# Kernel optimization log

Measured on AMD Instinct MI355X. Metric: run time of the kernel, lower is better.

Reference implementation:

```python
import jax, jax.numpy as jnp
import numpy as np

B = 128; RES = 28; DIM = 192; HEADS = 6; WS = 7; HDIM = DIM // HEADS
NWIN = (RES // WS) ** 2; N = WS * WS; SCALE = HDIM ** -0.5

def _rel_pos_index():
    coords = np.stack(np.meshgrid(np.arange(WS), np.arange(WS), indexing='ij'))
    cf = coords.reshape(2, -1)
    rel = (cf[:, :, None] - cf[:, None, :]).transpose(1, 2, 0)
    rel[:, :, 0] += WS - 1; rel[:, :, 1] += WS - 1; rel[:, :, 0] *= 2 * WS - 1
    return jnp.asarray(rel.sum(-1))

RPI = _rel_pos_index()  # (49,49) int32

def gelu(x):
    return jax.nn.gelu(x, approximate=False)  # torch nn.GELU default (erf)

def ln(x, g, b, eps=1e-5):
    mu = jnp.mean(x, -1, keepdims=True)
    var = jnp.var(x, -1, keepdims=True)
    return (x - mu) * jax.lax.rsqrt(var + eps) * g + b

def feat_extract(x, dw, se1, se2, pw):
    # x: (B,C,H,W). depthwise3x3 -> GELU -> SE -> pointwise, residual, maxpool s2
    y = jax.lax.conv_general_dilated(x, dw, (1, 1), [(1, 1), (1, 1)],
                                     feature_group_count=DIM,
                                     dimension_numbers=('NCHW', 'OIHW', 'NCHW'))
    y = gelu(y)
    s = jnp.mean(y, (2, 3))                       # squeeze-excite
    s = jax.nn.sigmoid(gelu(s @ se1.T) @ se2.T)
    y = y * s[:, :, None, None]
    y = jax.lax.conv_general_dilated(y, pw, (1, 1), [(0, 0), (0, 0)],
                                     dimension_numbers=('NCHW', 'OIHW', 'NCHW'))
    x = x + y
    return jax.lax.reduce_window(x, -jnp.inf, jax.lax.max,
                                 (1, 1, 3, 3), (1, 1, 2, 2),
                                 [(0, 0), (0, 0), (1, 1), (1, 1)])

def win_part(x):
    b = x.shape[0]
    x = x.reshape(b, RES // WS, WS, RES // WS, WS, DIM).transpose(0, 1, 3, 2, 4, 5)
    return x.reshape(-1, N, DIM)

def win_rev(w, b):
    x = w.reshape(b, RES // WS, RES // WS, WS, WS, DIM).transpose(0, 1, 3, 2, 4, 5)
    return x.reshape(b, RES, RES, DIM)

def rel_bias(rpb):
    return jnp.take(rpb, RPI.reshape(-1), axis=0).reshape(N, N, HEADS).transpose(2, 0, 1)[None]

def attn_block(x, q_global, n1g, n1b, qkv_w, qkv_b, rpb, proj_w, proj_b,
               n2g, n2b, fc1w, fc1b, fc2w, fc2b, is_global):
    b = x.shape[0]
    xw = win_part(ln(x, n1g, n1b))                # (b*NWIN, N, C)
    B_ = xw.shape[0]
    if is_global:
        kv = (xw @ qkv_w.T + qkv_b).reshape(B_, N, 2, HEADS, HDIM).transpose(2, 0, 3, 1, 4)
        k, v = kv[0], kv[1]
        q = jnp.broadcast_to(q_global, (b, NWIN, HEADS, N, HDIM)).reshape(B_, HEADS, N, HDIM) * SCALE
    else:
        qkv = (xw @ qkv_w.T + qkv_b).reshape(B_, N, 3, HEADS, HDIM).transpose(2, 0, 3, 1, 4)
        q, k, v = qkv[0] * SCALE, qkv[1], qkv[2]
    attn = jnp.einsum('bhnd,bhmd->bhnm', q, k) + rel_bias(rpb)
    attn = jax.nn.softmax(attn, axis=-1)
    o = jnp.einsum('bhnm,bhmd->bhnd', attn, v).transpose(0, 2, 1, 3).reshape(B_, N, DIM)
    o = o @ proj_w.T + proj_b
    x = x + win_rev(o, b)
    h = ln(x, n2g, n2b)
    h = gelu(h @ fc1w.T + fc1b) @ fc2w.T + fc2b
    return x + h

def _forward(x, fe0_dw, fe0_se1, fe0_se2, fe0_pw, fe1_dw, fe1_se1, fe1_se2, fe1_pw,
             b0_n1g, b0_n1b, b0_qkv_w, b0_qkv_b, b0_rpb, b0_proj_w, b0_proj_b,
             b0_n2g, b0_n2b, b0_fc1w, b0_fc1b, b0_fc2w, b0_fc2b,
             b1_n1g, b1_n1b, b1_qkv_w, b1_qkv_b, b1_rpb, b1_proj_w, b1_proj_b,
             b1_n2g, b1_n2b, b1_fc1w, b1_fc1b, b1_fc2w, b1_fc2b):
    b = x.shape[0]
    # GlobalQueryGen: channel-first, two FeatExtract downsamples 28->14->7
    xc = jnp.transpose(x, (0, 3, 1, 2))
    xc = feat_extract(xc, fe0_dw, fe0_se1, fe0_se2, fe0_pw)
    xc = feat_extract(xc, fe1_dw, fe1_se1, fe1_se2, fe1_pw)
    qg = jnp.transpose(xc, (0, 2, 3, 1)).reshape(b, 1, N, HEADS, HDIM).transpose(0, 1, 3, 2, 4)
    # block 0: local window attention; block 1: global-query window attention
    x = attn_block(x, None, b0_n1g, b0_n1b, b0_qkv_w, b0_qkv_b, b0_rpb, b0_proj_w,
                   b0_proj_b, b0_n2g, b0_n2b, b0_fc1w, b0_fc1b, b0_fc2w, b0_fc2b, False)
    x = attn_block(x, qg, b1_n1g, b1_n1b, b1_qkv_w, b1_qkv_b, b1_rpb, b1_proj_w,
                   b1_proj_b, b1_n2g, b1_n2b, b1_fc1w, b1_fc1b, b1_fc2w, b1_fc2b, True)
    return x

def setup_inputs() -> dict:
    key = jax.random.key(0)
    ks = iter(jax.random.split(key, 64))
    r = lambda *s: jax.random.normal(next(ks), s, jnp.float32) * 0.02
    d = {'x': jax.random.normal(next(ks), (B, RES, RES, DIM), jnp.float32)}
    for i in range(2):
        d[f'fe{i}_dw'] = r(DIM, 1, 3, 3)
        d[f'fe{i}_se1'] = r(DIM // 4, DIM)
        d[f'fe{i}_se2'] = r(DIM, DIM // 4)
        d[f'fe{i}_pw'] = r(DIM, DIM, 1, 1)
    for i, qm in ((0, 3), (1, 2)):  # local: qkv, global: kv only
        p = f'b{i}_'
        d[p + 'n1g'] = jnp.ones(DIM, jnp.float32); d[p + 'n1b'] = jnp.zeros(DIM, jnp.float32)
        d[p + 'qkv_w'] = r(qm * DIM, DIM); d[p + 'qkv_b'] = r(qm * DIM)
        d[p + 'rpb'] = r((2 * WS - 1) ** 2, HEADS)
        d[p + 'proj_w'] = r(DIM, DIM); d[p + 'proj_b'] = r(DIM)
        d[p + 'n2g'] = jnp.ones(DIM, jnp.float32); d[p + 'n2b'] = jnp.zeros(DIM, jnp.float32)
        d[p + 'fc1w'] = r(4 * DIM, DIM); d[p + 'fc1b'] = r(4 * DIM)
        d[p + 'fc2w'] = r(DIM, 4 * DIM); d[p + 'fc2b'] = r(DIM)
    return d

def reference(x, fe0_dw, fe0_se1, fe0_se2, fe0_pw, fe1_dw, fe1_se1, fe1_se2, fe1_pw,
              b0_n1g, b0_n1b, b0_qkv_w, b0_qkv_b, b0_rpb, b0_proj_w, b0_proj_b,
              b0_n2g, b0_n2b, b0_fc1w, b0_fc1b, b0_fc2w, b0_fc2b,
              b1_n1g, b1_n1b, b1_qkv_w, b1_qkv_b, b1_rpb, b1_proj_w, b1_proj_b,
              b1_n2g, b1_n2b, b1_fc1w, b1_fc1b, b1_fc2w, b1_fc2b):
    return _forward(x, fe0_dw, fe0_se1, fe0_se2, fe0_pw, fe1_dw, fe1_se1, fe1_se2, fe1_pw,
                    b0_n1g, b0_n1b, b0_qkv_w, b0_qkv_b, b0_rpb, b0_proj_w, b0_proj_b,
                    b0_n2g, b0_n2b, b0_fc1w, b0_fc1b, b0_fc2w, b0_fc2b,
                    b1_n1g, b1_n1b, b1_qkv_w, b1_qkv_b, b1_rpb, b1_proj_w, b1_proj_b,
                    b1_n2g, b1_n2b, b1_fc1w, b1_fc1b, b1_fc2w, b1_fc2b)
```

## Files before the change

kernel.cpp:

```cpp
#include <hip/hip_runtime.h>
#include <hip/hip_bf16.h>
#include <math.h>

#define NB     128
#define RESX   28
#define DIMC   192
#define NHEADS 6
#define WSZ    7
#define HD     32
#define NTOK   49
#define SCALE  0.17677669529663687f
#define TOK28  (NB*RESX*RESX)
#define QSTR   208
#define VSTR   80
#define PSTR   80
#define HSTR   200
#define SEPARTS 8

typedef short    bf16x8 __attribute__((ext_vector_type(8)));
typedef float    f32x4  __attribute__((ext_vector_type(4)));

__device__ __forceinline__ float gelu_f(float x){
    return 0.5f * x * (1.0f + erff(x * 0.70710678118654752f));
}
__device__ __forceinline__ unsigned short f2bf(float f){
    unsigned int u = __float_as_uint(f);
    u += 0x7fffu + ((u >> 16) & 1u);
    return (unsigned short)(u >> 16);
}
__device__ __forceinline__ float bf2f(unsigned short u){
    return __uint_as_float(((unsigned int)u) << 16);
}
__device__ __forceinline__ bf16x8 pack8(float4 u, float4 v){
    bf16x8 r;
    r[0]=(short)f2bf(u.x); r[1]=(short)f2bf(u.y); r[2]=(short)f2bf(u.z); r[3]=(short)f2bf(u.w);
    r[4]=(short)f2bf(v.x); r[5]=(short)f2bf(v.y); r[6]=(short)f2bf(v.z); r[7]=(short)f2bf(v.w);
    return r;
}

__global__ __launch_bounds__(256) void ln_kernel(const float* __restrict__ x,
        const float* __restrict__ g, const float* __restrict__ be,
        float* __restrict__ out)
{
    int wid = threadIdx.x >> 6, lane = threadIdx.x & 63;
    size_t tok = (size_t)blockIdx.x * 4 + wid;
    const float* xr = x + tok * DIMC;
    float v0 = xr[lane], v1 = xr[lane + 64], v2 = xr[lane + 128];
    float s  = v0 + v1 + v2;
    float sq = v0*v0 + v1*v1 + v2*v2;
    #pragma unroll
    for (int o = 32; o > 0; o >>= 1){ s += __shfl_xor(s, o); sq += __shfl_xor(sq, o); }
    float mean = s * (1.0f/DIMC);
    float var  = sq * (1.0f/DIMC) - mean*mean;
    float rstd = rsqrtf(var + 1e-5f);
    float* orow = out + tok * DIMC;
    orow[lane]     = (v0-mean)*rstd*g[lane]     + be[lane];
    orow[lane+64]  = (v1-mean)*rstd*g[lane+64]  + be[lane+64];
    orow[lane+128] = (v2-mean)*rstd*g[lane+128] + be[lane+128];
}

__global__ __launch_bounds__(192) void dw_gelu_kernel(const float* __restrict__ x,
        const float* __restrict__ dw, float* __restrict__ y, int H, int W)
{
    __shared__ float wl[DIMC*9];
    int tx = threadIdx.x;
    #pragma unroll
    for (int q = 0; q < 9; ++q) wl[tx*9 + q] = dw[tx*9 + q];
    __syncthreads();
    int pix = tx / 48, c4 = tx - (tx/48)*48;
    int p = blockIdx.x*4 + pix;
    int w = p % W; int h = (p / W) % H; int b = p / (W*H);
    float wk[9][4];
    #pragma unroll
    for (int q = 0; q < 9; ++q){
        #pragma unroll
        for (int cc = 0; cc < 4; ++cc) wk[q][cc] = wl[(c4*4 + cc)*9 + q];
    }
    const float* base = x + (size_t)b*H*W*DIMC + c4*4;
    float4 acc = make_float4(0.f, 0.f, 0.f, 0.f);
    #pragma unroll
    for (int kh = 0; kh < 3; ++kh){
        int hh = h + kh - 1; if (hh < 0 || hh >= H) continue;
        #pragma unroll
        for (int kw = 0; kw < 3; ++kw){
            int ww = w + kw - 1; if (ww < 0 || ww >= W) continue;
            float4 v = *(const float4*)(base + ((size_t)hh*W + ww)*DIMC);
            int q = kh*3 + kw;
            acc.x += v.x*wk[q][0]; acc.y += v.y*wk[q][1];
            acc.z += v.z*wk[q][2]; acc.w += v.w*wk[q][3];
        }
    }
    float4 o;
    o.x = gelu_f(acc.x); o.y = gelu_f(acc.y);
    o.z = gelu_f(acc.z); o.w = gelu_f(acc.w);
    *(float4*)(y + (size_t)p*DIMC + c4*4) = o;
}

__global__ void se_reduce_kernel(const float* __restrict__ y, float* __restrict__ part,
                                 int HW)
{
    int blk = blockIdx.x;
    int b = blk / SEPARTS, i = blk - b*SEPARTS;
    int c = threadIdx.x;
    int chunk = (HW + SEPARTS - 1) / SEPARTS;
    int p0 = i*chunk, p1 = p0 + chunk;
    if (p1 > HW) p1 = HW;
    const float* base = y + (size_t)b*HW*DIMC + c;
    float acc = 0.f;
    for (int p = p0; p < p1; ++p) acc += base[(size_t)p*DIMC];
    part[(size_t)blk*DIMC + c] = acc;
}

__global__ void se_mlp_kernel(const float* __restrict__ part, const float* __restrict__ w1,
                              const float* __restrict__ w2, float* __restrict__ s, int HW)
{
    __shared__ float sl[DIMC];
    __shared__ float mid[48];
    int b = blockIdx.x; int t = threadIdx.x;
    float acc0 = 0.f;
    #pragma unroll
    for (int i = 0; i < SEPARTS; ++i)
        acc0 += part[((size_t)b*SEPARTS + i)*DIMC + t];
    sl[t] = acc0 / (float)HW;
    __syncthreads();
    if (t < 48){
        float acc = 0.f;
        for (int c = 0; c < DIMC; ++c) acc += sl[c] * w1[t*DIMC + c];
        mid[t] = gelu_f(acc);
    }
    __syncthreads();
    float acc = 0.f;
    #pragma unroll 8
    for (int j = 0; j < 48; ++j) acc += mid[j] * w2[t*48 + j];
    s[b*DIMC + t] = 1.0f / (1.0f + expf(-acc));
}

__global__ __launch_bounds__(192) void maxpool_kernel(const float* __restrict__ x,
        float* __restrict__ out, int H, int W)
{
    int H2 = H >> 1, W2 = W >> 1;
    int tx = threadIdx.x;
    int pix = tx / 48, c4 = tx - (tx/48)*48;
    int p = blockIdx.x*4 + pix;
    if (p >= NB*H2*W2) return;
    int w2 = p % W2; int h2 = (p / W2) % H2; int b = p / (W2*H2);
    const float* base = x + (size_t)b*H*W*DIMC + c4*4;
    float4 m = make_float4(-INFINITY, -INFINITY, -INFINITY, -INFINITY);
    #pragma unroll
    for (int dh = -1; dh <= 1; ++dh){
        int h = 2*h2 + dh; if (h < 0 || h >= H) continue;
        #pragma unroll
        for (int dw = -1; dw <= 1; ++dw){
            int w = 2*w2 + dw; if (w < 0 || w >= W) continue;
            float4 v = *(const float4*)(base + ((size_t)h*W + w)*DIMC);
            m.x = fmaxf(m.x, v.x); m.y = fmaxf(m.y, v.y);
            m.z = fmaxf(m.z, v.z); m.w = fmaxf(m.w, v.w);
        }
    }
    *(float4*)(out + (size_t)p*DIMC + c4*4) = m;
}

struct PackArgs {
    const float* src[8];
    unsigned short* dst[8];
    int K[8];
    int tEnd[8];
    int nseg;
};
__global__ __launch_bounds__(256) void pack_multi_kernel(PackArgs a)
{
    int t = blockIdx.x*256 + threadIdx.x;
    int seg = 0;
    while (seg < a.nseg && t >= a.tEnd[seg]) ++seg;
    if (seg >= a.nseg) return;
    int t0 = seg ? a.tEnd[seg-1] : 0;
    int tl = t - t0;
    int lane = tl & 63, frag = tl >> 6;
    int K = a.K[seg], ks = K >> 5;
    int j = frag / ks, s = frag - j*ks;
    const float* wr = a.src[seg] + (size_t)(j*16 + (lane & 15))*K + s*32 + ((lane>>4)<<3);
    bf16x8 r = pack8(*(const float4*)wr, *(const float4*)(wr + 4));
    *((bf16x8*)(a.dst[seg] + (size_t)tl*8)) = r;
}

__global__ __launch_bounds__(256) void gemmW_kernel(
    const float* __restrict__ in, const unsigned short* __restrict__ Wp,
    const float* __restrict__ bias, const float* __restrict__ res,
    float* __restrict__ out, int N, int M, int ppw,
    const float* __restrict__ sv, int HW)
{
    __shared__ __align__(16) unsigned short wlds[72*512];
    __shared__ __align__(16) float sbias[192];
    int tid = threadIdx.x;
    int l = tid & 63, w = tid >> 6, c = l & 15, g = l >> 4;
    int nc = blockIdx.y;
    const bf16x8* wsrc = (const bf16x8*)(Wp + (size_t)nc*36864);
    bf16x8* wdst = (bf16x8*)wlds;
    #pragma unroll 2
    for (int i = tid; i < 4608; i += 256) wdst[i] = wsrc[i];
    if (tid < 48){
        float4 bb = bias ? ((const float4*)(bias + nc*192))[tid]
                         : make_float4(0.f,0.f,0.f,0.f);
        ((float4*)sbias)[tid] = bb;
    }
    __syncthreads();
    size_t mbase = (size_t)blockIdx.x*(128*ppw) + (size_t)w*(32*ppw);
    for (int p = 0; p < ppw; ++p){
        size_t m0 = mbase + (size_t)p*32;
        if ((long)m0 >= M) break;
        bool st1 = (long)(m0 + 16) < M;
        const float* ar0 = in + (m0 + c)*DIMC;
        const float* ar1 = ar0 + 16*DIMC;
        bf16x8 b0[6], b1[6];
        #pragma unroll
        for (int s = 0; s < 6; ++s){
            int k0 = s*32 + g*8;
            float4 u0 = *(const float4*)(ar0 + k0), v0 = *(const float4*)(ar0 + k0 + 4);
            float4 u1 = *(const float4*)(ar1 + k0), v1 = *(const float4*)(ar1 + k0 + 4);
            if (sv){
                int bi0 = (int)((m0 + c)/HW), bi1 = (int)((m0 + 16 + c)/HW);
                float4 a0 = *(const float4*)(sv + (size_t)bi0*DIMC + k0);
                float4 a1 = *(const float4*)(sv + (size_t)bi0*DIMC + k0 + 4);
                float4 d0 = *(const float4*)(sv + (size_t)bi1*DIMC + k0);
                float4 d1 = *(const float4*)(sv + (size_t)bi1*DIMC + k0 + 4);
                u0.x*=a0.x; u0.y*=a0.y; u0.z*=a0.z; u0.w*=a0.w;
                v0.x*=a1.x; v0.y*=a1.y; v0.z*=a1.z; v0.w*=a1.w;
                u1.x*=d0.x; u1.y*=d0.y; u1.z*=d0.z; u1.w*=d0.w;
                v1.x*=d1.x; v1.y*=d1.y; v1.z*=d1.z; v1.w*=d1.w;
            }
            b0[s] = pack8(u0, v0);
            b1[s] = pack8(u1, v1);
        }
        #pragma unroll 2
        for (int j = 0; j < 12; ++j){
            float4 bb = *(const float4*)(sbias + j*16 + g*4);
            f32x4 a0 = {bb.x, bb.y, bb.z, bb.w};
            f32x4 a1 = a0;
            const bf16x8* wf = (const bf16x8*)wlds + (size_t)j*6*64 + l;
            #pragma unroll
            for (int s = 0; s < 6; ++s){
                bf16x8 wfr = wf[s*64];
                a0 = __builtin_amdgcn_mfma_f32_16x16x32_bf16(wfr, b0[s], a0, 0, 0, 0);
                a1 = __builtin_amdgcn_mfma_f32_16x16x32_bf16(wfr, b1[s], a1, 0, 0, 0);
            }
            int ncol = nc*192 + j*16 + g*4;
            size_t o0 = (m0 + c)*(size_t)N + ncol;
            size_t o1 = o0 + (size_t)16*N;
            float4 r0 = res ? *(const float4*)(res + o0) : make_float4(0.f,0.f,0.f,0.f);
            *(float4*)(out + o0) = make_float4(a0[0]+r0.x, a0[1]+r0.y, a0[2]+r0.z, a0[3]+r0.w);
            if (st1){
                float4 r1 = res ? *(const float4*)(res + o1) : make_float4(0.f,0.f,0.f,0.f);
                *(float4*)(out + o1) = make_float4(a1[0]+r1.x, a1[1]+r1.y, a1[2]+r1.z, a1[3]+r1.w);
            }
        }
    }
}

__global__ __launch_bounds__(256, 2) void mlp_mfma_kernel(
    const float* __restrict__ xln,
    const unsigned short* __restrict__ W1p, const float* __restrict__ b1,
    const unsigned short* __restrict__ W2p, const float* __restrict__ b2,
    float* __restrict__ xout)
{
    __shared__ __align__(16) unsigned short h[2][64*HSTR];
    int l = threadIdx.x & 63, w = threadIdx.x >> 6;
    int c = l & 15, g = l >> 4;
    size_t m0 = (size_t)blockIdx.x*64;
    bf16x8 bx[4][6];
    #pragma unroll
    for (int mt = 0; mt < 4; ++mt){
        const float* ar = xln + (m0 + mt*16 + c)*DIMC;
        #pragma unroll
        for (int s = 0; s < 6; ++s){
            int k0 = s*32 + g*8;
            bx[mt][s] = pack8(*(const float4*)(ar + k0), *(const float4*)(ar + k0 + 4));
        }
    }
    f32x4 acc[4][3];
    #pragma unroll
    for (int jj = 0; jj < 3; ++jj){
        float4 b4 = *(const float4*)(b2 + (3*w + jj)*16 + g*4);
        f32x4 v = {b4.x, b4.y, b4.z, b4.w};
        #pragma unroll
        for (int mt = 0; mt < 4; ++mt) acc[mt][jj] = v;
    }
    for (int ch = 0; ch < 4; ++ch){
        unsigned short* hb = &h[ch & 1][0];
        #pragma unroll
        for (int jj = 0; jj < 3; ++jj){
            int j = ch*12 + 3*w + jj;
            float4 b40 = *(const float4*)(b1 + j*16 + g*4);
            f32x4 a0 = {b40.x, b40.y, b40.z, b40.w};
            f32x4 a1 = a0, a2 = a0, a3 = a0;
            const bf16x8* wp = (const bf16x8*)(W1p + ((size_t)(j*6)*64 + l)*8);
            #pragma unroll
            for (int s = 0; s < 6; ++s){
                bf16x8 wfr = wp[s*64];
                a0 = __builtin_amdgcn_mfma_f32_16x16x32_bf16(wfr, bx[0][s], a0, 0, 0, 0);
                a1 = __builtin_amdgcn_mfma_f32_16x16x32_bf16(wfr, bx[1][s], a1, 0, 0, 0);
                a2 = __builtin_amdgcn_mfma_f32_16x16x32_bf16(wfr, bx[2][s], a2, 0, 0, 0);
                a3 = __builtin_amdgcn_mfma_f32_16x16x32_bf16(wfr, bx[3][s], a3, 0, 0, 0);
            }
            int fb = (3*w + jj)*16 + g*4;
            ushort4 u;
            u.x=f2bf(gelu_f(a0[0])); u.y=f2bf(gelu_f(a0[1]));
            u.z=f2bf(gelu_f(a0[2])); u.w=f2bf(gelu_f(a0[3]));
            *(ushort4*)(hb + (0*16 + c)*HSTR + fb) = u;
            u.x=f2bf(gelu_f(a1[0])); u.y=f2bf(gelu_f(a1[1]));
            u.z=f2bf(gelu_f(a1[2])); u.w=f2bf(gelu_f(a1[3]));
            *(ushort4*)(hb + (1*16 + c)*HSTR + fb) = u;
            u.x=f2bf(gelu_f(a2[0])); u.y=f2bf(gelu_f(a2[1]));
            u.z=f2bf(gelu_f(a2[2])); u.w=f2bf(gelu_f(a2[3]));
            *(ushort4*)(hb + (2*16 + c)*HSTR + fb) = u;
            u.x=f2bf(gelu_f(a3[0])); u.y=f2bf(gelu_f(a3[1]));
            u.z=f2bf(gelu_f(a3[2])); u.w=f2bf(gelu_f(a3[3]));
            *(ushort4*)(hb + (3*16 + c)*HSTR + fb) = u;
        }
        __syncthreads();
        #pragma unroll
        for (int s = 0; s < 6; ++s){
            bf16x8 hf[4];
            #pragma unroll
            for (int mt = 0; mt < 4; ++mt)
                hf[mt] = *(const bf16x8*)(hb + (mt*16 + c)*HSTR + s*32 + g*8);
            #pragma unroll
            for (int jj = 0; jj < 3; ++jj){
                int j = 3*w + jj;
                bf16x8 wf = *(const bf16x8*)(W2p + ((size_t)(j*24 + ch*6 + s)*64 + l)*8);
                #pragma unroll
                for (int mt = 0; mt < 4; ++mt)
                    acc[mt][jj] = __builtin_amdgcn_mfma_f32_16x16x32_bf16(wf, hf[mt], acc[mt][jj], 0, 0, 0);
            }
        }
    }
    #pragma unroll
    for (int mt = 0; mt < 4; ++mt){
        #pragma unroll
        for (int jj = 0; jj < 3; ++jj){
            size_t o = (m0 + mt*16 + c)*DIMC + (3*w + jj)*16 + g*4;
            float4 r = *(const float4*)(xout + o);
            *(float4*)(xout + o) = make_float4(acc[mt][jj][0]+r.x, acc[mt][jj][1]+r.y,
                                               acc[mt][jj][2]+r.z, acc[mt][jj][3]+r.w);
        }
    }
}

__global__ __launch_bounds__(512, 2) void attn_fused_kernel(
    float* __restrict__ xio, const unsigned short* __restrict__ Wp,
    const float* __restrict__ bias, const float* __restrict__ qg,
    const float* __restrict__ rpb, int F)
{
    __shared__ __align__(16) unsigned short q_lds[64*QSTR];
    __shared__ __align__(16) unsigned short k_lds[64*QSTR];
    __shared__ __align__(16) unsigned short vt[192*VSTR];
    __shared__ __align__(16) unsigned short pp[8*16*PSTR];
    __shared__ float sinv_l[8*16];
    __shared__ float rpb_l[NHEADS*169];
    int tid = threadIdx.x;
    int w8 = tid >> 6;
    int l = tid & 63, c = l & 15, g = l >> 4;
    int blk = blockIdx.x;
    int b = blk >> 4, win = blk & 15;
    int wr = win >> 2, wc = win & 3;
    bool isglobal = (F == 384);

    for (int i = tid; i < 15*QSTR; i += 512){
        q_lds[49*QSTR + i] = 0; k_lds[49*QSTR + i] = 0;
    }
    for (int i = tid; i < 192*15; i += 512){
        int d = i / 15, t = 49 + (i - d*15);
        vt[d*VSTR + t] = 0;
    }
    for (int i = tid; i < NHEADS*169; i += 512){
        int hd = i / 169, r = i - hd*169;
        rpb_l[i] = rpb[r*NHEADS + hd];
    }

    {
        bf16x8 bx[4][6];
        #pragma unroll
        for (int mt = 0; mt < 4; ++mt){
            int t = mt*16 + c;
            if (t < NTOK){
                int hh = wr*WSZ + t/WSZ, ww = wc*WSZ + t - (t/WSZ)*WSZ;
                const float* ar = xio + (((size_t)b*RESX + hh)*RESX + ww)*DIMC;
                #pragma unroll
                for (int s = 0; s < 6; ++s){
                    int k0 = s*32 + g*8;
                    bx[mt][s] = pack8(*(const float4*)(ar + k0), *(const float4*)(ar + k0 + 4));
                }
            } else {
                bf16x8 z = {0,0,0,0,0,0,0,0};
                #pragma unroll
                for (int s = 0; s < 6; ++s) bx[mt][s] = z;
            }
        }
        int ntile = F >> 4;
        for (int jn = w8; jn < ntile; jn += 8){
            float4 bb4 = *(const float4*)(bias + jn*16 + g*4);
            f32x4 a0 = {bb4.x, bb4.y, bb4.z, bb4.w};
            f32x4 a1 = a0, a2 = a0, a3 = a0;
            const bf16x8* wp = (const bf16x8*)(Wp + ((size_t)(jn*6)*64 + l)*8);
            #pragma unroll
            for (int s = 0; s < 6; ++s){
                bf16x8 wfr = wp[s*64];
                a0 = __builtin_amdgcn_mfma_f32_16x16x32_bf16(wfr, bx[0][s], a0, 0, 0, 0);
                a1 = __builtin_amdgcn_mfma_f32_16x16x32_bf16(wfr, bx[1][s], a1, 0, 0, 0);
                a2 = __builtin_amdgcn_mfma_f32_16x16x32_bf16(wfr, bx[2][s], a2, 0, 0, 0);
                a3 = __builtin_amdgcn_mfma_f32_16x16x32_bf16(wfr, bx[3][s], a3, 0, 0, 0);
            }
            int sect = jn / 12 + (isglobal ? 1 : 0);
            int frel = (jn - (jn/12)*12)*16 + g*4;
            f32x4 av[4] = {a0, a1, a2, a3};
            #pragma unroll
            for (int mt = 0; mt < 4; ++mt){
                int t = mt*16 + c;
                if (t >= NTOK) continue;
                f32x4 a = av[mt];
                if (sect == 0){
                    ushort4 u;
                    u.x=f2bf(a[0]*SCALE); u.y=f2bf(a[1]*SCALE);
                    u.z=f2bf(a[2]*SCALE); u.w=f2bf(a[3]*SCALE);
                    *(ushort4*)(q_lds + t*QSTR + frel) = u;
                } else if (sect == 1){
                    ushort4 u;
                    u.x=f2bf(a[0]); u.y=f2bf(a[1]); u.z=f2bf(a[2]); u.w=f2bf(a[3]);
                    *(ushort4*)(k_lds + t*QSTR + frel) = u;
                } else {
                    vt[(frel+0)*VSTR + t] = f2bf(a[0]);
                    vt[(frel+1)*VSTR + t] = f2bf(a[1]);
                    vt[(frel+2)*VSTR + t] = f2bf(a[2]);
                    vt[(frel+3)*VSTR + t] = f2bf(a[3]);
                }
            }
        }
        if (isglobal){
            for (int i = tid; i < NTOK*48; i += 512){
                int t = i / 48, f4 = i - (i/48)*48;
                float4 qv = *(const float4*)(qg + ((size_t)b*NTOK + t)*DIMC + f4*4);
                ushort4 u;
                u.x=f2bf(qv.x*SCALE); u.y=f2bf(qv.y*SCALE);
                u.z=f2bf(qv.z*SCALE); u.w=f2bf(qv.w*SCALE);
                *(ushort4*)(q_lds + t*QSTR + f4*4) = u;
            }
        }
    }
    __syncthreads();

    for (int uu = 0; uu < 3; ++uu){
        int unit = w8*3 + uu;
        int ti = unit / 6, hd = unit - (unit/6)*6;
        bf16x8 qa = *(const bf16x8*)(q_lds + (16*ti + c)*QSTR + hd*HD + g*8);
        f32x4 S[4];
        {
            const f32x4 z = {0.f, 0.f, 0.f, 0.f};
            __builtin_amdgcn_s_setprio(1);
            #pragma unroll
            for (int tj = 0; tj < 4; ++tj){
                bf16x8 kb = *(const bf16x8*)(k_lds + (16*tj + c)*QSTR + hd*HD + g*8);
                S[tj] = __builtin_amdgcn_mfma_f32_16x16x32_bf16(qa, kb, z, 0, 0, 0);
            }
            __builtin_amdgcn_s_setprio(0);
        }
        float tot[4] = {0.f, 0.f, 0.f, 0.f};
        unsigned short pu[4][4];
        int ibase = 16*ti + g*4;
        #pragma unroll
        for (int tj = 0; tj < 4; ++tj){
            int j = 16*tj + c;
            bool jok = (j < NTOK);
            int jc = jok ? j : 0;
            int rj = jc / 7, cj = jc - rj*7;
            #pragma unroll
            for (int r = 0; r < 4; ++r){
                int i = ibase + r;
                int ic = (i < NTOK) ? i : 0;
                int ri = ic / 7, ci = ic - ri*7;
                unsigned short u16 = 0;
                if (jok){
                    float bv = rpb_l[hd*169 + (ri - rj + 6)*13 + (ci - cj + 6)];
                    u16 = f2bf(__expf(S[tj][r] + bv));
                }
                pu[tj][r] = u16;
                tot[r] += bf2f(u16);
            }
        }
        #pragma unroll
        for (int r = 0; r < 4; ++r){
            float t0 = tot[r];
            t0 += __shfl_xor(t0, 1); t0 += __shfl_xor(t0, 2);
            t0 += __shfl_xor(t0, 4); t0 += __shfl_xor(t0, 8);
            tot[r] = t0;
        }
        if (c == 0){
            #pragma unroll
            for (int r = 0; r < 4; ++r)
                sinv_l[w8*16 + g*4 + r] = 1.0f / tot[r];
        }
        #pragma unroll
        for (int tj = 0; tj < 4; ++tj){
            #pragma unroll
            for (int r = 0; r < 4; ++r)
                pp[(w8*16 + g*4 + r)*PSTR + 16*tj + c] = pu[tj][r];
        }
        bf16x8 pb0 = *(const bf16x8*)(pp + (w8*16 + c)*PSTR + g*8);
        bf16x8 pb1 = *(const bf16x8*)(pp + (w8*16 + c)*PSTR + 32 + g*8);
        float si = sinv_l[w8*16 + c];
        int t = 16*ti + c;
        #pragma unroll
        for (int dm = 0; dm < 2; ++dm){
            int vrow = hd*HD + dm*16 + c;
            bf16x8 va0 = *(const bf16x8*)(vt + vrow*VSTR + g*8);
            bf16x8 va1 = *(const bf16x8*)(vt + vrow*VSTR + 32 + g*8);
            const f32x4 z = {0.f, 0.f, 0.f, 0.f};
            __builtin_amdgcn_s_setprio(1);
            f32x4 o = __builtin_amdgcn_mfma_f32_16x16x32_bf16(va0, pb0, z, 0, 0, 0);
            o = __builtin_amdgcn_mfma_f32_16x16x32_bf16(va1, pb1, o, 0, 0, 0);
            __builtin_amdgcn_s_setprio(0);
            if (t < NTOK){
                int hh = wr*WSZ + t/WSZ, ww = wc*WSZ + t - (t/WSZ)*WSZ;
                float4 ov = make_float4(o[0]*si, o[1]*si, o[2]*si, o[3]*si);
                *(float4*)(xio + (((size_t)b*RESX + hh)*RESX + ww)*DIMC
                           + hd*HD + dm*16 + g*4) = ov;
            }
        }
    }
}

static inline int pick_ppw(int M){
    int ppw = M / 65536;
    if (ppw < 1) ppw = 1;
    if (ppw > 8) ppw = 8;
    return ppw;
}

extern "C" void kernel_launch(void* const* d_in, const int* in_sizes, int n_in,
                              void* d_out, int out_size, void* d_ws, size_t ws_size,
                              hipStream_t stream)
{
    (void)in_sizes; (void)n_in; (void)out_size;
    const float* x = (const float*)d_in[0];
    const float* fe_dw[2]  = {(const float*)d_in[1], (const float*)d_in[5]};
    const float* fe_se1[2] = {(const float*)d_in[2], (const float*)d_in[6]};
    const float* fe_se2[2] = {(const float*)d_in[3], (const float*)d_in[7]};
    const float* fe_pw[2]  = {(const float*)d_in[4], (const float*)d_in[8]};
    const float* n1g[2]  = {(const float*)d_in[9],  (const float*)d_in[22]};
    const float* n1b[2]  = {(const float*)d_in[10], (const float*)d_in[23]};
    const float* qkvw[2] = {(const float*)d_in[11], (const float*)d_in[24]};
    const float* qkvb[2] = {(const float*)d_in[12], (const float*)d_in[25]};
    const float* rpb[2]  = {(const float*)d_in[13], (const float*)d_in[26]};
    const float* prjw[2] = {(const float*)d_in[14], (const float*)d_in[27]};
    const float* prjb[2] = {(const float*)d_in[15], (const float*)d_in[28]};
    const float* n2g[2]  = {(const float*)d_in[16], (const float*)d_in[29]};
    const float* n2b[2]  = {(const float*)d_in[17], (const float*)d_in[30]};
    const float* fc1w[2] = {(const float*)d_in[18], (const float*)d_in[31]};
    const float* fc1b[2] = {(const float*)d_in[19], (const float*)d_in[32]};
    const float* fc2w[2] = {(const float*)d_in[20], (const float*)d_in[33]};
    const float* fc2b[2] = {(const float*)d_in[21], (const float*)d_in[34]};

    float* out = (float*)d_out;
    float* ws = (float*)d_ws;
    const size_t n28 = (size_t)NB*RESX*RESX*DIMC;
    const size_t n14 = (size_t)NB*14*14*DIMC;
    const size_t n7  = (size_t)NB*7*7*DIMC;
    float* region0 = ws;
    float* x7      = region0 + n28;
    float* s0      = x7 + n7;
    float* s1      = s0 + NB*DIMC;
    float* pwpk_f  = s1 + NB*DIMC;
    float* dyn     = pwpk_f + 36864;
    size_t fixedf  = n28 + n7 + 2ull*NB*DIMC + 36864;
    if (ws_size < (fixedf + n14) * sizeof(float)) return;
    float* x14 = dyn;
    unsigned short* pwpk = (unsigned short*)pwpk_f;

    unsigned short* pk = (unsigned short*)dyn;
    const size_t PK_QKV0 = 0;
    const size_t PK_QKV1 = PK_QKV0 + 576*192;
    const size_t PK_PRJ0 = PK_QKV1 + 384*192;
    const size_t PK_PRJ1 = PK_PRJ0 + 192*192;
    const size_t PK_FC10 = PK_PRJ1 + 192*192;
    const size_t PK_FC11 = PK_FC10 + 768*192;
    const size_t PK_FC20 = PK_FC11 + 768*192;
    const size_t PK_FC21 = PK_FC20 + 192*768;

    {
        PackArgs a = {};
        a.src[0] = fe_pw[0]; a.dst[0] = pwpk;         a.K[0] = 192; a.tEnd[0] = 4608;
        a.src[1] = fe_pw[1]; a.dst[1] = pwpk + 36864; a.K[1] = 192; a.tEnd[1] = 9216;
        a.nseg = 2;
        pack_multi_kernel<<<(9216 + 255)/256, 256, 0, stream>>>(a);
    }

    for (int fe = 0; fe < 2; ++fe){
        int H = fe ? 14 : 28;
        int HW = H * H;
        int M = NB * HW;
        const float* src = fe ? x14 : x;
        float* dst = fe ? x7 : x14;
        dw_gelu_kernel<<<NB*HW/4, 192, 0, stream>>>(src, fe_dw[fe], region0, H, H);
        se_reduce_kernel<<<NB*SEPARTS, DIMC, 0, stream>>>(region0, x7, HW);
        se_mlp_kernel<<<NB, DIMC, 0, stream>>>(x7, fe_se1[fe], fe_se2[fe], s1, HW);
        int ppw = pick_ppw(M);
        dim3 ga((M + 128*ppw - 1) / (128*ppw), 1);
        gemmW_kernel<<<ga, 256, 0, stream>>>(region0, pwpk + fe*36864, nullptr,
                                             src, region0, DIMC, M, ppw, s1, HW);
        int npool = NB*(H/2)*(H/2);
        maxpool_kernel<<<(npool + 3)/4, 192, 0, stream>>>(region0, dst, H, H);
    }

    {
        PackArgs a = {};
        const float* srcs[8] = {qkvw[0], qkvw[1], prjw[0], prjw[1],
                                fc1w[0], fc1w[1], fc2w[0], fc2w[1]};
        size_t offs[8] = {PK_QKV0, PK_QKV1, PK_PRJ0, PK_PRJ1,
                          PK_FC10, PK_FC11, PK_FC20, PK_FC21};
        int kk[8]  = {192, 192, 192, 192, 192, 192, 768, 768};
        int cnt[8] = {13824, 9216, 4608, 4608, 18432, 18432, 18432, 18432};
        int cum = 0;
        for (int i = 0; i < 8; ++i){
            a.src[i] = srcs[i]; a.dst[i] = pk + offs[i]; a.K[i] = kk[i];
            cum += cnt[i]; a.tEnd[i] = cum;
        }
        a.nseg = 8;
        pack_multi_kernel<<<(cum + 255)/256, 256, 0, stream>>>(a);
    }

    for (int blk = 0; blk < 2; ++blk){
        const float* xin = blk ? (const float*)out : x;
        ln_kernel<<<TOK28/4, 256, 0, stream>>>(xin, n1g[blk], n1b[blk], region0);
        int F = blk ? 384 : 576;
        attn_fused_kernel<<<NB*16, 512, 0, stream>>>(
            region0, pk + (blk ? PK_QKV1 : PK_QKV0), qkvb[blk],
            blk ? x7 : nullptr, rpb[blk], F);
        {
            int M = TOK28;
            int ppw = pick_ppw(M);
            dim3 gp((M + 128*ppw - 1) / (128*ppw), 1);
            gemmW_kernel<<<gp, 256, 0, stream>>>(region0,
                pk + (blk ? PK_PRJ1 : PK_PRJ0), prjb[blk], xin, out,
                DIMC, M, ppw, nullptr, 0);
        }
        ln_kernel<<<TOK28/4, 256, 0, stream>>>(out, n2g[blk], n2b[blk], region0);
        mlp_mfma_kernel<<<TOK28/64, 256, 0, stream>>>(region0,
            pk + (blk ? PK_FC11 : PK_FC10), fc1b[blk],
            pk + (blk ? PK_FC21 : PK_FC20), fc2b[blk], out);
    }
}
```

Measured before the change: 1.120 ms.

## Fuse output projection, residual add and second LayerNorm into attention kernel

The attention output is now kept in LDS as bf16 instead of being written to global memory in fp32. The same block then runs the projection GEMM with MFMA, adds the residual, and applies the pre-MLP LayerNorm for its own window tokens. This removes the separate projection GEMM launch and LayerNorm launch, along with the global round-trips of the intermediate activations. In exchange the kernel uses extra LDS and an uneven 12-tile split across 8 waves. The LayerNorm also reads back just-written global output and writes into the same buffer it read its input from.

```diff
diff --git a/kernel.cpp b/kernel.cpp
--- a/kernel.cpp
+++ b/kernel.cpp
@@ -346,14 +346,18 @@
 }
 
 __global__ __launch_bounds__(512, 2) void attn_fused_kernel(
-    float* __restrict__ xio, const unsigned short* __restrict__ Wp,
-    const float* __restrict__ bias, const float* __restrict__ qg,
-    const float* __restrict__ rpb, int F)
+    const float* __restrict__ xln, const float* __restrict__ xin,
+    float* __restrict__ outg, float* __restrict__ lnout,
+    const unsigned short* __restrict__ Wp, const float* __restrict__ bias,
+    const unsigned short* __restrict__ Pw, const float* __restrict__ pbias,
+    const float* __restrict__ qg, const float* __restrict__ rpb,
+    const float* __restrict__ lng, const float* __restrict__ lnb, int F)
 {
     __shared__ __align__(16) unsigned short q_lds[64*QSTR];
     __shared__ __align__(16) unsigned short k_lds[64*QSTR];
     __shared__ __align__(16) unsigned short vt[192*VSTR];
     __shared__ __align__(16) unsigned short pp[8*16*PSTR];
+    __shared__ __align__(16) unsigned short obuf[64*QSTR];
     __shared__ float sinv_l[8*16];
     __shared__ float rpb_l[NHEADS*169];
     int tid = threadIdx.x;
@@ -365,7 +369,7 @@
     bool isglobal = (F == 384);
 
     for (int i = tid; i < 15*QSTR; i += 512){
-        q_lds[49*QSTR + i] = 0; k_lds[49*QSTR + i] = 0;
+        q_lds[49*QSTR + i] = 0; k_lds[49*QSTR + i] = 0; obuf[49*QSTR + i] = 0;
     }
     for (int i = tid; i < 192*15; i += 512){
         int d = i / 15, t = 49 + (i - d*15);
@@ -383,7 +387,7 @@
             int t = mt*16 + c;
             if (t < NTOK){
                 int hh = wr*WSZ + t/WSZ, ww = wc*WSZ + t - (t/WSZ)*WSZ;
-                const float* ar = xio + (((size_t)b*RESX + hh)*RESX + ww)*DIMC;
+                const float* ar = xln + (((size_t)b*RESX + hh)*RESX + ww)*DIMC;
                 #pragma unroll
                 for (int s = 0; s < 6; ++s){
                     int k0 = s*32 + g*8;
@@ -518,12 +522,66 @@
             o = __builtin_amdgcn_mfma_f32_16x16x32_bf16(va1, pb1, o, 0, 0, 0);
             __builtin_amdgcn_s_setprio(0);
             if (t < NTOK){
+                ushort4 u;
+                u.x=f2bf(o[0]*si); u.y=f2bf(o[1]*si);
+                u.z=f2bf(o[2]*si); u.w=f2bf(o[3]*si);
+                *(ushort4*)(obuf + t*QSTR + hd*HD + dm*16 + g*4) = u;
+            }
+        }
+    }
+    __syncthreads();
+
+    {
+        bf16x8 ox[4][6];
+        #pragma unroll
+        for (int mt = 0; mt < 4; ++mt){
+            #pragma unroll
+            for (int s = 0; s < 6; ++s)
+                ox[mt][s] = *(const bf16x8*)(obuf + (mt*16 + c)*QSTR + s*32 + g*8);
+        }
+        for (int jn = w8; jn < 12; jn += 8){
+            float4 bb4 = *(const float4*)(pbias + jn*16 + g*4);
+            f32x4 a0 = {bb4.x, bb4.y, bb4.z, bb4.w};
+            f32x4 a1 = a0, a2 = a0, a3 = a0;
+            const bf16x8* wp = (const bf16x8*)(Pw + ((size_t)(jn*6)*64 + l)*8);
+            #pragma unroll
+            for (int s = 0; s < 6; ++s){
+                bf16x8 wfr = wp[s*64];
+                a0 = __builtin_amdgcn_mfma_f32_16x16x32_bf16(wfr, ox[0][s], a0, 0, 0, 0);
+                a1 = __builtin_amdgcn_mfma_f32_16x16x32_bf16(wfr, ox[1][s], a1, 0, 0, 0);
+                a2 = __builtin_amdgcn_mfma_f32_16x16x32_bf16(wfr, ox[2][s], a2, 0, 0, 0);
+                a3 = __builtin_amdgcn_mfma_f32_16x16x32_bf16(wfr, ox[3][s], a3, 0, 0, 0);
+            }
+            f32x4 av[4] = {a0, a1, a2, a3};
+            #pragma unroll
+            for (int mt = 0; mt < 4; ++mt){
+                int t = mt*16 + c;
+                if (t >= NTOK) continue;
                 int hh = wr*WSZ + t/WSZ, ww = wc*WSZ + t - (t/WSZ)*WSZ;
-                float4 ov = make_float4(o[0]*si, o[1]*si, o[2]*si, o[3]*si);
-                *(float4*)(xio + (((size_t)b*RESX + hh)*RESX + ww)*DIMC
-                           + hd*HD + dm*16 + g*4) = ov;
-            }
-        }
+                size_t po = (((size_t)b*RESX + hh)*RESX + ww)*DIMC + jn*16 + g*4;
+                float4 r = *(const float4*)(xin + po);
+                f32x4 a = av[mt];
+                *(float4*)(outg + po) = make_float4(a[0]+r.x, a[1]+r.y, a[2]+r.z, a[3]+r.w);
+            }
+        }
+    }
+    __syncthreads();
+
+    for (int t = w8; t < NTOK; t += 8){
+        int hh = wr*WSZ + t/WSZ, ww = wc*WSZ + t - (t/WSZ)*WSZ;
+        size_t ro = (((size_t)b*RESX + hh)*RESX + ww)*DIMC;
+        float v0 = outg[ro + l], v1 = outg[ro + l + 64], v2 = outg[ro + l + 128];
+        float s = v0 + v1 + v2;
+        float sq = v0*v0 + v1*v1 + v2*v2;
+        #pragma unroll
+        for (int o2 = 32; o2 > 0; o2 >>= 1){
+            s += __shfl_xor(s, o2); sq += __shfl_xor(sq, o2);
+        }
+        float mean = s * (1.0f/DIMC);
+        float rstd = rsqrtf(sq * (1.0f/DIMC) - mean*mean + 1e-5f);
+        lnout[ro + l]       = (v0-mean)*rstd*lng[l]       + lnb[l];
+        lnout[ro + l + 64]  = (v1-mean)*rstd*lng[l + 64]  + lnb[l + 64];
+        lnout[ro + l + 128] = (v2-mean)*rstd*lng[l + 128] + lnb[l + 128];
     }
 }
 
@@ -631,17 +689,10 @@
         ln_kernel<<<TOK28/4, 256, 0, stream>>>(xin, n1g[blk], n1b[blk], region0);
         int F = blk ? 384 : 576;
         attn_fused_kernel<<<NB*16, 512, 0, stream>>>(
-            region0, pk + (blk ? PK_QKV1 : PK_QKV0), qkvb[blk],
-            blk ? x7 : nullptr, rpb[blk], F);
-        {
-            int M = TOK28;
-            int ppw = pick_ppw(M);
-            dim3 gp((M + 128*ppw - 1) / (128*ppw), 1);
-            gemmW_kernel<<<gp, 256, 0, stream>>>(region0,
-                pk + (blk ? PK_PRJ1 : PK_PRJ0), prjb[blk], xin, out,
-                DIMC, M, ppw, nullptr, 0);
-        }
-        ln_kernel<<<TOK28/4, 256, 0, stream>>>(out, n2g[blk], n2b[blk], region0);
+            region0, xin, out, region0,
+            pk + (blk ? PK_QKV1 : PK_QKV0), qkvb[blk],
+            pk + (blk ? PK_PRJ1 : PK_PRJ0), prjb[blk],
+            blk ? x7 : nullptr, rpb[blk], n2g[blk], n2b[blk], F);
         mlp_mfma_kernel<<<TOK28/64, 256, 0, stream>>>(region0,
             pk + (blk ? PK_FC11 : PK_FC10), fc1b[blk],
             pk + (blk ? PK_FC21 : PK_FC20), fc2b[blk], out);
```

After: 1.125 ms. About the same (+0.5%).
